# Performance work log

Measured on AMD Instinct MI355X. Metric: run time of the kernel, lower is better.

Reference implementation:

```python
import jax, jax.numpy as jnp
import numpy as np

V, D, T, H = 32000, 1024, 1024, 16
HD = D // H  # head_size = 64
B = 4


def setup_inputs() -> dict:
    key = jax.random.key(0)
    ks = jax.random.split(key, 12)
    s = 0.02
    return {
        "idx": jax.random.randint(ks[0], (B, T), 0, V),
        "tok_emb": jax.random.normal(ks[1], (V, D), jnp.float32) * s,
        "pos_emb": jax.random.normal(ks[2], (T, D), jnp.float32) * s,
        "Wq": jax.random.normal(ks[3], (H, D, HD), jnp.float32) * s,
        "Wk": jax.random.normal(ks[4], (H, D, HD), jnp.float32) * s,
        "Wv": jax.random.normal(ks[5], (H, D, HD), jnp.float32) * s,
        "W1": jax.random.normal(ks[6], (D, D), jnp.float32) * s,
        "b1": jnp.zeros((D,), jnp.float32),
        "W2": jax.random.normal(ks[7], (D, D), jnp.float32) * s,
        "b2": jnp.zeros((D,), jnp.float32),
        "Wout": jax.random.normal(ks[8], (D, V), jnp.float32) * s,
        "bout": jnp.zeros((V,), jnp.float32),
    }


def reference(idx, tok_emb, pos_emb, Wq, Wk, Wv, W1, b1, W2, b2, Wout, bout):
    t = idx.shape[1]
    x = tok_emb[idx] + pos_emb[:t]  # [B,T,D]
    # per-head q,k,v projections (no bias), vectorized over heads
    q = jnp.einsum("btd,hde->bhte", x, Wq)
    k = jnp.einsum("btd,hde->bhte", x, Wk)
    v = jnp.einsum("btd,hde->bhte", x, Wv)
    scores = jnp.einsum("bhte,bhse->bhts", q, k) / jnp.sqrt(jnp.float32(HD))
    causal = jnp.tril(jnp.ones((t, t), bool))
    scores = jnp.where(causal, scores, -jnp.inf)
    w = jax.nn.softmax(scores, axis=-1)
    att = jnp.einsum("bhts,bhse->bhte", w, v)  # [B,H,T,HD]
    # concat heads along feature dim -> [B,T,D]
    out = att.transpose(0, 2, 1, 3).reshape(idx.shape[0], t, D)
    h = jax.nn.relu(out @ W1 + b1)
    h = jax.nn.relu(h @ W2 + b2)
    logits = h @ Wout + bout  # [B,T,V]
    return logits
```

## Files before the change

### kernel.cpp

```cpp
#include <hip/hip_runtime.h>
#include <cstdint>
#include <cstddef>


#define DEV __device__ __forceinline__

typedef __attribute__((ext_vector_type(8))) short bf16x8;
typedef __attribute__((ext_vector_type(4))) float f32x4;

DEV unsigned short f2bf(float f) {
  unsigned u = __float_as_uint(f);
  u = (u + 0x7fffu + ((u >> 16) & 1u)) >> 16;
  return (unsigned short)u;
}

DEV void stage16(const void* g, void* l) {
  __builtin_amdgcn_global_load_lds(
      (const __attribute__((address_space(1))) unsigned int*)g,
      (__attribute__((address_space(3))) unsigned int*)l, 16, 0, 0);
}

__global__ __launch_bounds__(256) void k_embed(
    const int* __restrict__ idx, const float* __restrict__ tok,
    const float* __restrict__ pos, unsigned short* __restrict__ xb) {
  int i = blockIdx.x * 256 + threadIdx.x;
  int row = i >> 8;
  int c4 = i & 255;
  int t = row & 1023;
  int tokid = idx[row];
  const float4 a = ((const float4*)tok)[(size_t)tokid * 256 + c4];
  const float4 p = ((const float4*)pos)[(size_t)t * 256 + c4];
  ushort4 o;
  o.x = f2bf(a.x + p.x); o.y = f2bf(a.y + p.y);
  o.z = f2bf(a.z + p.z); o.w = f2bf(a.w + p.w);
  ((ushort4*)xb)[i] = o;
}

__global__ __launch_bounds__(256) void k_pack_qkv(
    const float* __restrict__ Wq, const float* __restrict__ Wk,
    const float* __restrict__ Wv, unsigned short* __restrict__ out) {
  __shared__ float tile[64][65];
  int blk = blockIdx.x;
  int p = blk >> 8, h = (blk >> 4) & 15, d0 = (blk & 15) * 64;
  const float* W = (p == 0) ? Wq : ((p == 1) ? Wk : Wv);
  int tid = threadIdx.x, rq = tid >> 6, cc = tid & 63;
#pragma unroll
  for (int it = 0; it < 16; ++it) {
    int dr = it * 4 + rq;
    tile[dr][cc] = W[((size_t)h * 1024 + d0 + dr) * 64 + cc];
  }
  __syncthreads();
#pragma unroll
  for (int it = 0; it < 16; ++it) {
    int e = it * 4 + rq;
    out[((size_t)(p * 1024 + h * 64 + e)) * 1024 + d0 + cc] = f2bf(tile[cc][e]);
  }
}

__global__ __launch_bounds__(256) void k_transpose(
    const float* __restrict__ in, unsigned short* __restrict__ out,
    int R, int C) {
  __shared__ float tile[64][65];
  int c0 = blockIdx.x * 64, r0 = blockIdx.y * 64;
  int tid = threadIdx.x, rq = tid >> 6, cc = tid & 63;
#pragma unroll
  for (int it = 0; it < 16; ++it) {
    int r = it * 4 + rq;
    tile[r][cc] = in[(size_t)(r0 + r) * C + c0 + cc];
  }
  __syncthreads();
#pragma unroll
  for (int it = 0; it < 16; ++it) {
    int c = it * 4 + rq;
    out[(size_t)(c0 + c) * R + r0 + cc] = f2bf(tile[cc][c]);
  }
}

template <int EP>
__global__ __launch_bounds__(256) void k_gemm(
    const unsigned short* __restrict__ A, const unsigned short* __restrict__ Bt,
    const float* __restrict__ bias, void* __restrict__ out0,
    void* __restrict__ out1, void* __restrict__ out2, int M, int N, int K) {
  __shared__ __align__(16) unsigned short As[128 * 32];
  __shared__ __align__(16) unsigned short Bs[128 * 32];
  const int tid = threadIdx.x;
  const int lane = tid & 63, w = tid >> 6;
  const int wr = w >> 1, wc = w & 1;
  const int fr = lane & 15, fg = lane >> 4;
  const int m0 = blockIdx.y * 128, n0 = blockIdx.x * 128;
  const int pch = (fg ^ ((fr >> 1) & 3)) << 3;

  f32x4 zero = {0.f, 0.f, 0.f, 0.f};
  f32x4 acc[4][4];
#pragma unroll
  for (int m = 0; m < 4; ++m)
#pragma unroll
    for (int n = 0; n < 4; ++n) acc[m][n] = zero;

  const int srow = tid >> 2;
  const int sch = (((tid & 3) ^ ((srow >> 1) & 3))) * 8;
  const unsigned short* Ab0 = A + (size_t)(m0 + srow) * K + sch;
  const unsigned short* Ab1 = A + (size_t)(m0 + 64 + srow) * K + sch;
  const unsigned short* Bb0 = Bt + (size_t)(n0 + srow) * K + sch;
  const unsigned short* Bb1 = Bt + (size_t)(n0 + 64 + srow) * K + sch;
  unsigned short* Ad0 = &As[tid * 8];
  unsigned short* Ad1 = &As[(tid + 256) * 8];
  unsigned short* Bd0 = &Bs[tid * 8];
  unsigned short* Bd1 = &Bs[(tid + 256) * 8];

  for (int k0 = 0; k0 < K; k0 += 32) {
    stage16(Ab0 + k0, Ad0);
    stage16(Ab1 + k0, Ad1);
    stage16(Bb0 + k0, Bd0);
    stage16(Bb1 + k0, Bd1);
    __syncthreads();
    bf16x8 af[4], bfv[4];
#pragma unroll
    for (int m = 0; m < 4; ++m)
      af[m] = *(const bf16x8*)&As[(wr * 64 + m * 16 + fr) * 32 + pch];
#pragma unroll
    for (int n = 0; n < 4; ++n)
      bfv[n] = *(const bf16x8*)&Bs[(wc * 64 + n * 16 + fr) * 32 + pch];
#pragma unroll
    for (int m = 0; m < 4; ++m)
#pragma unroll
      for (int n = 0; n < 4; ++n)
        acc[m][n] = __builtin_amdgcn_mfma_f32_16x16x32_bf16(af[m], bfv[n],
                                                            acc[m][n], 0, 0, 0);
    __syncthreads();
  }

#pragma unroll
  for (int m = 0; m < 4; ++m) {
#pragma unroll
    for (int n = 0; n < 4; ++n) {
      const int rb = m0 + wr * 64 + m * 16 + fg * 4;
      const int cc = n0 + wc * 64 + n * 16 + fr;
#pragma unroll
      for (int i = 0; i < 4; ++i) {
        float v = acc[m][n][i];
        const int r = rb + i;
        if (EP == 1) {
          v += bias[cc];
          v = v > 0.f ? v : 0.f;
          ((unsigned short*)out0)[(size_t)r * N + cc] = f2bf(v);
        } else if (EP == 3) {
          int p = cc >> 10, rem = cc & 1023;
          int h = rem >> 6, e = rem & 63;
          int b = r >> 10, t = r & 1023;
          unsigned short* dst =
              (p == 0) ? (unsigned short*)out0
                       : ((p == 1) ? (unsigned short*)out1 : (unsigned short*)out2);
          dst[(((size_t)(b * 16 + h) * 1024) + t) * 64 + e] = f2bf(v);
        }
      }
    }
  }
}

__global__ __launch_bounds__(512, 2) void k_gemm256(
    const unsigned short* __restrict__ A, const unsigned short* __restrict__ Bt,
    const float* __restrict__ bias, float* __restrict__ out,
    int M, int N, int K) {
  __shared__ __align__(16) unsigned short sm[4 * 16384];
  const int tid = threadIdx.x;
  const int lane = tid & 63, wid = tid >> 6;
  const int wr = wid >> 2, wc = wid & 3;
  const int fr = lane & 15, fg = lane >> 4;
  const int pch = (fg ^ ((fr >> 1) & 3)) << 3;

  const int nwg = gridDim.x * gridDim.y;
  int wg = blockIdx.y * gridDim.x + blockIdx.x;
  if ((nwg & 7) == 0) wg = (wg & 7) * (nwg >> 3) + (wg >> 3);
  const int m0 = (wg % gridDim.y) * 256;
  const int n0 = (wg / gridDim.y) * 256;

  const int srow = tid >> 2;
  const int scol = (((tid & 3) ^ ((srow >> 1) & 3))) * 8;
  const int NT = K >> 5;

#define STAGE_A(t, bb)                                                      \
  do {                                                                      \
    const unsigned short* g = A + (size_t)(m0 + srow) * K + (t) * 32 + scol; \
    stage16(g, &sm[(bb) * 16384 + tid * 8]);                                \
    stage16(g + (size_t)128 * K, &sm[(bb) * 16384 + 4096 + tid * 8]);       \
  } while (0)
#define STAGE_B(t, bb)                                                      \
  do {                                                                      \
    const unsigned short* g = Bt + (size_t)(n0 + srow) * K + (t) * 32 + scol; \
    stage16(g, &sm[(bb) * 16384 + 8192 + tid * 8]);                         \
    stage16(g + (size_t)128 * K, &sm[(bb) * 16384 + 8192 + 4096 + tid * 8]); \
  } while (0)

  f32x4 zero = {0.f, 0.f, 0.f, 0.f};
  f32x4 acc[8][4];
#pragma unroll
  for (int m = 0; m < 8; ++m)
#pragma unroll
    for (int n = 0; n < 4; ++n) acc[m][n] = zero;

  STAGE_A(0, 0); STAGE_B(0, 0);
  STAGE_A(1, 1); STAGE_B(1, 1);
  STAGE_A(2, 2); STAGE_B(2, 2);
  asm volatile("s_waitcnt vmcnt(8)" ::: "memory");
  __builtin_amdgcn_s_barrier();

  for (int t = 0; t < NT; ++t) {
    const unsigned short* Ab = &sm[(t & 3) * 16384];
    const unsigned short* Bb = &sm[(t & 3) * 16384 + 8192];
    const bool pre = (t + 3) < NT;
    const int bpre = (t + 3) & 3;

    bf16x8 af0[4], bfv[4];
#pragma unroll
    for (int m = 0; m < 4; ++m)
      af0[m] = *(const bf16x8*)&Ab[(wr * 128 + m * 16 + fr) * 32 + pch];
#pragma unroll
    for (int n = 0; n < 4; ++n)
      bfv[n] = *(const bf16x8*)&Bb[(wc * 64 + n * 16 + fr) * 32 + pch];
    if (pre) STAGE_A(t + 3, bpre);
    __builtin_amdgcn_s_barrier();
    asm volatile("s_waitcnt lgkmcnt(0)" ::: "memory");
    __builtin_amdgcn_sched_barrier(0);
    __builtin_amdgcn_s_setprio(1);
#pragma unroll
    for (int m = 0; m < 4; ++m)
#pragma unroll
      for (int n = 0; n < 4; ++n)
        acc[m][n] = __builtin_amdgcn_mfma_f32_16x16x32_bf16(af0[m], bfv[n],
                                                            acc[m][n], 0, 0, 0);
    __builtin_amdgcn_s_setprio(0);
    __builtin_amdgcn_s_barrier();

    bf16x8 af1[4];
#pragma unroll
    for (int m = 0; m < 4; ++m)
      af1[m] = *(const bf16x8*)&Ab[(wr * 128 + (m + 4) * 16 + fr) * 32 + pch];
    if (pre) STAGE_B(t + 3, bpre);
    __builtin_amdgcn_s_barrier();
    asm volatile("s_waitcnt lgkmcnt(0)" ::: "memory");
    __builtin_amdgcn_sched_barrier(0);
    __builtin_amdgcn_s_setprio(1);
#pragma unroll
    for (int m = 0; m < 4; ++m)
#pragma unroll
      for (int n = 0; n < 4; ++n)
        acc[m + 4][n] = __builtin_amdgcn_mfma_f32_16x16x32_bf16(
            af1[m], bfv[n], acc[m + 4][n], 0, 0, 0);
    __builtin_amdgcn_s_setprio(0);
    if (t + 3 < NT) {
      asm volatile("s_waitcnt vmcnt(8)" ::: "memory");
    } else if (t + 2 < NT) {
      asm volatile("s_waitcnt vmcnt(4)" ::: "memory");
    } else {
      asm volatile("s_waitcnt vmcnt(0)" ::: "memory");
    }
    __builtin_amdgcn_s_barrier();
  }
#undef STAGE_A
#undef STAGE_B

#pragma unroll
  for (int m = 0; m < 8; ++m) {
#pragma unroll
    for (int n = 0; n < 4; ++n) {
      const int rb = m0 + wr * 128 + m * 16 + fg * 4;
      const int cc = n0 + wc * 64 + n * 16 + fr;
      const float bs = bias[cc];
#pragma unroll
      for (int i = 0; i < 4; ++i)
        __builtin_nontemporal_store(acc[m][n][i] + bs,
                                    &out[(size_t)(rb + i) * N + cc]);
    }
  }
}

__global__ __launch_bounds__(256) void k_attn(
    const unsigned short* __restrict__ qb, const unsigned short* __restrict__ kb,
    const unsigned short* __restrict__ vb, unsigned short* __restrict__ attx) {
  __shared__ __align__(16) unsigned short Klds[64][72];
  __shared__ __align__(16) unsigned short Vt[64][72];
  __shared__ __align__(16) unsigned short Plds[4][16][72];
  const int qt = blockIdx.x;
  const int bh = blockIdx.y;
  const int tid = threadIdx.x;
  const int w = tid >> 6, lane = tid & 63;
  const int fr = lane & 15, g = lane >> 4;
  const size_t base = (size_t)bh * (1024 * 64);
  const int q0 = qt * 64 + w * 16;
  const int q_abs = q0 + fr;

  bf16x8 qf[2];
#pragma unroll
  for (int t = 0; t < 2; ++t)
    qf[t] = *(const bf16x8*)&qb[base + (size_t)(q0 + fr) * 64 + t * 32 + g * 8];

  f32x4 zero = {0.f, 0.f, 0.f, 0.f};
  f32x4 o[4];
#pragma unroll
  for (int hb = 0; hb < 4; ++hb) o[hb] = zero;
  float m_s = -3.0e38f, l_s = 0.f;

  for (int jt = 0; jt <= qt; ++jt) {
    const int kvb = jt * 64;
#pragma unroll
    for (int it = 0; it < 2; ++it) {
      int c = tid + it * 256;
      int r = c >> 3, e0 = (c & 7) * 8;
      uint4 kd = *(const uint4*)&kb[base + (size_t)(kvb + r) * 64 + e0];
      *(uint4*)&Klds[r][e0] = kd;
      uint4 vd = *(const uint4*)&vb[base + (size_t)(kvb + r) * 64 + e0];
      const unsigned short* vs = (const unsigned short*)&vd;
#pragma unroll
      for (int j = 0; j < 8; ++j) Vt[e0 + j][r] = vs[j];
    }
    __syncthreads();

    f32x4 st[4];
#pragma unroll
    for (int f = 0; f < 4; ++f) {
      st[f] = zero;
#pragma unroll
      for (int t = 0; t < 2; ++t) {
        bf16x8 kf = *(const bf16x8*)&Klds[f * 16 + fr][t * 32 + g * 8];
        st[f] = __builtin_amdgcn_mfma_f32_16x16x32_bf16(kf, qf[t], st[f], 0, 0, 0);
      }
    }
    float sv[4][4];
    float tm = -3.0e38f;
#pragma unroll
    for (int f = 0; f < 4; ++f)
#pragma unroll
      for (int i = 0; i < 4; ++i) {
        int kv = kvb + f * 16 + g * 4 + i;
        float s = st[f][i] * 0.125f;
        if (kv > q_abs) s = -3.0e38f;
        sv[f][i] = s;
        tm = fmaxf(tm, s);
      }
    tm = fmaxf(tm, __shfl_xor(tm, 16));
    tm = fmaxf(tm, __shfl_xor(tm, 32));
    float mnew = fmaxf(m_s, tm);
    float scale = expf(m_s - mnew);
    float lsum = 0.f;
#pragma unroll
    for (int f = 0; f < 4; ++f)
#pragma unroll
      for (int i = 0; i < 4; ++i) {
        float pv = expf(sv[f][i] - mnew);
        lsum += pv;
        Plds[w][fr][f * 16 + g * 4 + i] = f2bf(pv);
      }
    lsum += __shfl_xor(lsum, 16);
    lsum += __shfl_xor(lsum, 32);
    l_s = l_s * scale + lsum;
    m_s = mnew;
#pragma unroll
    for (int i = 0; i < 4; ++i) {
      float sc = __shfl(scale, g * 4 + i);
#pragma unroll
      for (int hb = 0; hb < 4; ++hb) o[hb][i] *= sc;
    }
    __syncthreads();
#pragma unroll
    for (int t = 0; t < 2; ++t) {
      bf16x8 pf = *(const bf16x8*)&Plds[w][fr][t * 32 + g * 8];
#pragma unroll
      for (int hb = 0; hb < 4; ++hb) {
        bf16x8 vf = *(const bf16x8*)&Vt[hb * 16 + fr][t * 32 + g * 8];
        o[hb] = __builtin_amdgcn_mfma_f32_16x16x32_bf16(pf, vf, o[hb], 0, 0, 0);
      }
    }
    __syncthreads();
  }

  const float inv = 1.f / l_s;
  const int b = bh >> 4, h = bh & 15;
#pragma unroll
  for (int i = 0; i < 4; ++i) {
    float sc = __shfl(inv, g * 4 + i);
    int trow = q0 + g * 4 + i;
    size_t rowoff = ((size_t)(b * 1024 + trow)) * 1024 + h * 64;
#pragma unroll
    for (int hb = 0; hb < 4; ++hb)
      attx[rowoff + hb * 16 + fr] = f2bf(o[hb][i] * sc);
  }
}

extern "C" void kernel_launch(void* const* d_in, const int* in_sizes, int n_in,
                              void* d_out, int out_size, void* d_ws,
                              size_t ws_size, hipStream_t stream) {
  const int* idx = (const int*)d_in[0];
  const float* tok = (const float*)d_in[1];
  const float* pos = (const float*)d_in[2];
  const float* Wq = (const float*)d_in[3];
  const float* Wk = (const float*)d_in[4];
  const float* Wv = (const float*)d_in[5];
  const float* W1 = (const float*)d_in[6];
  const float* b1 = (const float*)d_in[7];
  const float* W2 = (const float*)d_in[8];
  const float* b2 = (const float*)d_in[9];
  const float* Wout = (const float*)d_in[10];
  const float* bout = (const float*)d_in[11];
  float* out = (float*)d_out;

  char* ws = (char*)d_ws;
  unsigned short* xb    = (unsigned short*)(ws + 0);
  unsigned short* wqkvT = (unsigned short*)(ws + 8388608);
  unsigned short* w1T   = (unsigned short*)(ws + 14680064);
  unsigned short* w2T   = (unsigned short*)(ws + 16777216);
  unsigned short* woutT = (unsigned short*)(ws + 18874368);
  unsigned short* qbuf  = (unsigned short*)(ws + 84410368);
  unsigned short* kbuf  = (unsigned short*)(ws + 92798976);
  unsigned short* vbuf  = (unsigned short*)(ws + 101187584);
  unsigned short* attx  = (unsigned short*)(ws + 109576192);
  unsigned short* h1    = (unsigned short*)(ws + 117964800);
  unsigned short* h2    = xb;

  k_embed<<<4096, 256, 0, stream>>>(idx, tok, pos, xb);
  k_pack_qkv<<<768, 256, 0, stream>>>(Wq, Wk, Wv, wqkvT);
  k_transpose<<<dim3(16, 16), 256, 0, stream>>>(W1, w1T, 1024, 1024);
  k_transpose<<<dim3(16, 16), 256, 0, stream>>>(W2, w2T, 1024, 1024);
  k_transpose<<<dim3(500, 16), 256, 0, stream>>>(Wout, woutT, 1024, 32000);

  k_gemm<3><<<dim3(24, 32), 256, 0, stream>>>(xb, wqkvT, nullptr, qbuf, kbuf,
                                              vbuf, 4096, 3072, 1024);
  k_attn<<<dim3(16, 64), 256, 0, stream>>>(qbuf, kbuf, vbuf, attx);
  k_gemm<1><<<dim3(8, 32), 256, 0, stream>>>(attx, w1T, b1, h1, nullptr,
                                             nullptr, 4096, 1024, 1024);
  k_gemm<1><<<dim3(8, 32), 256, 0, stream>>>(h1, w2T, b2, h2, nullptr, nullptr,
                                             4096, 1024, 1024);
  k_gemm256<<<dim3(125, 16), 512, 0, stream>>>(h2, woutT, bout, out, 4096,
                                               32000, 1024);
}
```

Baseline: 555.0 us.

## Double-buffer LDS fragment reads in registers and drop per-tile barriers in GEMM loop

Measured after the change: 531.0 us. 1.05x faster.

```diff
diff --git a/kernel.cpp b/kernel.cpp
--- a/kernel.cpp
+++ b/kernel.cpp
@@ -192,6 +192,50 @@
     stage16(g + (size_t)128 * K, &sm[(bb) * 16384 + 8192 + 4096 + tid * 8]); \
   } while (0)
 
+#define RD_G0(dA, dB, base)                                                 \
+  do {                                                                      \
+    _Pragma("unroll") for (int m_ = 0; m_ < 4; ++m_)                        \
+      dA[m_] = *(const bf16x8*)&(base)[(wr * 128 + m_ * 16 + fr) * 32 + pch]; \
+    _Pragma("unroll") for (int n_ = 0; n_ < 4; ++n_)                        \
+      dB[n_] = *(const bf16x8*)&(base)[8192 + (wc * 64 + n_ * 16 + fr) * 32 + pch]; \
+  } while (0)
+#define RD_AHI(dA, base)                                                    \
+  do {                                                                      \
+    _Pragma("unroll") for (int m_ = 0; m_ < 4; ++m_)                        \
+      dA[m_] = *(const bf16x8*)&(base)[(wr * 128 + (m_ + 4) * 16 + fr) * 32 + pch]; \
+  } while (0)
+
+#define MFMA_G(rbase, a, b)                                                 \
+  do {                                                                      \
+    __builtin_amdgcn_s_setprio(1);                                          \
+    _Pragma("unroll") for (int m_ = 0; m_ < 4; ++m_)                        \
+    _Pragma("unroll") for (int n_ = 0; n_ < 4; ++n_)                        \
+      acc[(rbase) + m_][n_] = __builtin_amdgcn_mfma_f32_16x16x32_bf16(      \
+          a[m_], b[n_], acc[(rbase) + m_][n_], 0, 0, 0);                    \
+    __builtin_amdgcn_s_setprio(0);                                          \
+  } while (0)
+
+#define TILE_BODY(t, curA, curB, nxtA, nxtB)                                \
+  do {                                                                      \
+    const unsigned short* Ab_ = &sm[((t) & 3) * 16384];                     \
+    bf16x8 a1_[4];                                                          \
+    RD_AHI(a1_, Ab_);                                                       \
+    if ((t) + 3 < NT) STAGE_A((t) + 3, ((t) + 3) & 3);                      \
+    MFMA_G(0, curA, curB);                                                  \
+    if ((t) + 1 < NT) {                                                     \
+      const unsigned short* An_ = &sm[(((t) + 1) & 3) * 16384];             \
+      RD_G0(nxtA, nxtB, An_);                                               \
+    }                                                                       \
+    if ((t) + 3 < NT) STAGE_B((t) + 3, ((t) + 3) & 3);                      \
+    MFMA_G(4, a1_, curB);                                                   \
+    if ((t) + 3 < NT) {                                                     \
+      asm volatile("s_waitcnt vmcnt(4)" ::: "memory");                      \
+    } else {                                                                \
+      asm volatile("s_waitcnt vmcnt(0)" ::: "memory");                      \
+    }                                                                       \
+    __builtin_amdgcn_s_barrier();                                           \
+  } while (0)
+
   f32x4 zero = {0.f, 0.f, 0.f, 0.f};
   f32x4 acc[8][4];
 #pragma unroll
@@ -202,63 +246,22 @@
   STAGE_A(0, 0); STAGE_B(0, 0);
   STAGE_A(1, 1); STAGE_B(1, 1);
   STAGE_A(2, 2); STAGE_B(2, 2);
-  asm volatile("s_waitcnt vmcnt(8)" ::: "memory");
+  asm volatile("s_waitcnt vmcnt(4)" ::: "memory");
   __builtin_amdgcn_s_barrier();
 
-  for (int t = 0; t < NT; ++t) {
-    const unsigned short* Ab = &sm[(t & 3) * 16384];
-    const unsigned short* Bb = &sm[(t & 3) * 16384 + 8192];
-    const bool pre = (t + 3) < NT;
-    const int bpre = (t + 3) & 3;
-
-    bf16x8 af0[4], bfv[4];
-#pragma unroll
-    for (int m = 0; m < 4; ++m)
-      af0[m] = *(const bf16x8*)&Ab[(wr * 128 + m * 16 + fr) * 32 + pch];
-#pragma unroll
-    for (int n = 0; n < 4; ++n)
-      bfv[n] = *(const bf16x8*)&Bb[(wc * 64 + n * 16 + fr) * 32 + pch];
-    if (pre) STAGE_A(t + 3, bpre);
-    __builtin_amdgcn_s_barrier();
-    asm volatile("s_waitcnt lgkmcnt(0)" ::: "memory");
-    __builtin_amdgcn_sched_barrier(0);
-    __builtin_amdgcn_s_setprio(1);
-#pragma unroll
-    for (int m = 0; m < 4; ++m)
-#pragma unroll
-      for (int n = 0; n < 4; ++n)
-        acc[m][n] = __builtin_amdgcn_mfma_f32_16x16x32_bf16(af0[m], bfv[n],
-                                                            acc[m][n], 0, 0, 0);
-    __builtin_amdgcn_s_setprio(0);
-    __builtin_amdgcn_s_barrier();
-
-    bf16x8 af1[4];
-#pragma unroll
-    for (int m = 0; m < 4; ++m)
-      af1[m] = *(const bf16x8*)&Ab[(wr * 128 + (m + 4) * 16 + fr) * 32 + pch];
-    if (pre) STAGE_B(t + 3, bpre);
-    __builtin_amdgcn_s_barrier();
-    asm volatile("s_waitcnt lgkmcnt(0)" ::: "memory");
-    __builtin_amdgcn_sched_barrier(0);
-    __builtin_amdgcn_s_setprio(1);
-#pragma unroll
-    for (int m = 0; m < 4; ++m)
-#pragma unroll
-      for (int n = 0; n < 4; ++n)
-        acc[m + 4][n] = __builtin_amdgcn_mfma_f32_16x16x32_bf16(
-            af1[m], bfv[n], acc[m + 4][n], 0, 0, 0);
-    __builtin_amdgcn_s_setprio(0);
-    if (t + 3 < NT) {
-      asm volatile("s_waitcnt vmcnt(8)" ::: "memory");
-    } else if (t + 2 < NT) {
-      asm volatile("s_waitcnt vmcnt(4)" ::: "memory");
-    } else {
-      asm volatile("s_waitcnt vmcnt(0)" ::: "memory");
-    }
-    __builtin_amdgcn_s_barrier();
+  bf16x8 xA[4], xB[4], yA[4], yB[4];
+  RD_G0(xA, xB, &sm[0]);
+
+  for (int t = 0; t < NT; t += 2) {
+    TILE_BODY(t, xA, xB, yA, yB);
+    TILE_BODY(t + 1, yA, yB, xA, xB);
   }
 #undef STAGE_A
 #undef STAGE_B
+#undef RD_G0
+#undef RD_AHI
+#undef MFMA_G
+#undef TILE_BODY
 
 #pragma unroll
   for (int m = 0; m < 8; ++m) {
```
